# Kernel optimization log

Hardware: AMD Instinct MI355X
Metric: run time of the kernel (lower is better)

## Reference

```python
import jax
import jax.numpy as jnp
import numpy as np

KSIZE, STRIDE, RATE, FUSE_K, SCALE = 3, 1, 2, 3, 10.0
ESCAPE_NAN = 1e-4


def _same_pad(x, k, s):
    # replicates torch same_padding: asymmetric zero pad so out = ceil(H/s)
    H, W = x.shape[2], x.shape[3]
    oh, ow = -(-H // s), -(-W // s)
    ph = max(0, (oh - 1) * s + k - H)
    pw = max(0, (ow - 1) * s + k - W)
    return jnp.pad(x, ((0, 0), (0, 0), (ph // 2, ph - ph // 2), (pw // 2, pw - pw // 2)))


def _extract_patches(x, k, s):
    # torch extract_image_patches: -> [B, L, C, k, k] with L = out_h*out_w
    x = _same_pad(x, k, s)
    B, C, H, W = x.shape
    Ho, Wo = (H - k) // s + 1, (W - k) // s + 1
    slices = [x[:, :, i:i + Ho * s:s, j:j + Wo * s:s] for i in range(k) for j in range(k)]
    p = jnp.stack(slices, axis=2).reshape(B, C, k, k, Ho, Wo)
    return p.transpose(0, 4, 5, 1, 2, 3).reshape(B, Ho * Wo, C, k, k)


def _contextual_attention(f, b, mask):
    dn = ('NCHW', 'OIHW', 'NCHW')
    # raw background patches for the final deconv: k = 2*rate, stride = rate
    raw_pat = _extract_patches(b, 2 * RATE, RATE * STRIDE)  # [B, L, C, 4, 4]
    # nearest-neighbor 1/rate downsample (torch F.interpolate nearest, sf=0.5)
    f_ds = f[:, :, ::RATE, ::RATE]
    b_ds = b[:, :, ::RATE, ::RATE]
    m_ds = mask[:, :, ::RATE, ::RATE]
    B, C, Hf, Wf = f_ds.shape
    Hb, Wb = b_ds.shape[2], b_ds.shape[3]
    b_pat = _extract_patches(b_ds, KSIZE, STRIDE)  # [B, L, C, 3, 3], L = Hb*Wb
    m_pat = _extract_patches(m_ds, KSIZE, STRIDE)[0]  # [L, 1, 3, 3] (first sample only, as in torch)
    mm = (jnp.mean(m_pat, axis=(1, 2, 3)) == 0.0).astype(f.dtype)[None, :, None, None]  # [1, L, 1, 1]
    fuse_w = jnp.eye(FUSE_K, dtype=f.dtype).reshape(1, 1, FUSE_K, FUSE_K)

    def per_item(xi, wi, raw_wi):
        # xi: [C,Hf,Wf]; wi: [L,C,3,3]; raw_wi: [L,C,4,4]
        max_wi = jnp.sqrt(jnp.sum(wi * wi + ESCAPE_NAN, axis=(1, 2, 3), keepdims=True))
        wi_n = wi / max_wi
        # matching conv: scores [1, L, Hf, Wf]
        yi = jax.lax.conv_general_dilated(xi[None], wi_n, (1, 1), ((1, 1), (1, 1)), dimension_numbers=dn)
        # fuse: identity-diagonal 3x3 conv along (bg_idx, fg_idx) twice with transposes
        yi = yi.reshape(1, 1, Hb * Wb, Hf * Wf)
        yi = jax.lax.conv_general_dilated(yi, fuse_w, (1, 1), ((1, 1), (1, 1)), dimension_numbers=dn)
        yi = yi.reshape(Hb, Wb, Hf, Wf).transpose(1, 0, 3, 2).reshape(1, 1, Hb * Wb, Hf * Wf)
        yi = jax.lax.conv_general_dilated(yi, fuse_w, (1, 1), ((1, 1), (1, 1)), dimension_numbers=dn)
        yi = yi.reshape(Wb, Hb, Wf, Hf).transpose(1, 0, 3, 2).reshape(1, Hb * Wb, Hf, Wf)
        yi = yi * mm
        yi = jax.nn.softmax(yi * SCALE, axis=1) * mm
        # conv_transpose2d(yi, raw_wi[I=L,O=C], stride=rate, padding=1) / 4
        w2 = jnp.flip(raw_wi, (2, 3)).transpose(1, 0, 2, 3)  # [C, L, 4, 4]
        pad = 2 * RATE - 1 - 1  # k - 1 - torch_padding = 2
        out = jax.lax.conv_general_dilated(yi, w2, (1, 1), ((pad, pad), (pad, pad)),
                                           lhs_dilation=(RATE, RATE), dimension_numbers=dn) / 4.0
        return out[0]

    return jax.vmap(per_item)(f_ds, b_pat, raw_pat)  # [B, C, H, W]


def setup_inputs() -> dict:
    key = jax.random.key(0)
    k1, k2 = jax.random.split(key)
    B, C, H, W = 2, 128, 128, 128
    f = jax.random.normal(k1, (B, C, H, W), dtype=jnp.float32)
    b = jax.random.normal(k2, (B, C, H, W), dtype=jnp.float32)
    mask = jnp.zeros((B, 1, H, W), dtype=jnp.float32)
    return {"f": f, "b": b, "mask": mask}


def reference(f, b, mask):
    return _contextual_attention(f, b, mask)
```

## Files before the change

kernel.cpp:

```cpp
#include <hip/hip_runtime.h>
#include <math.h>

#define CDIM 128
#define HF   128
#define WF   128
#define NP   4096
#define NCHUNK 64

typedef __attribute__((ext_vector_type(8))) short short8;
typedef __attribute__((ext_vector_type(16))) float f16a;
typedef float __attribute__((ext_vector_type(4), aligned(16))) f4a16;
typedef float __attribute__((ext_vector_type(4), aligned(4)))  f4u;

__device__ inline ushort f2bf(float x) {
  union { float f; unsigned u; } v; v.f = x;
  unsigned r = v.u + 0x7fff + ((v.u >> 16) & 1);
  return (ushort)(r >> 16);
}
__device__ inline float bf2f(ushort h) {
  union { unsigned u; float f; } v; v.u = ((unsigned)h) << 16; return v.f;
}

__device__ inline void gl2lds16(const ushort* g, ushort* l) {
  __builtin_amdgcn_global_load_lds((const __attribute__((address_space(1))) void*)g,
                                   (__attribute__((address_space(3))) void*)l, 16, 0, 0);
}

__global__ __launch_bounds__(256) void k_prep(const float* __restrict__ f,
                                              const float* __restrict__ b,
                                              ushort* __restrict__ fcat,
                                              ushort* __restrict__ bcat,
                                              float* __restrict__ s2) {
  int idx = blockIdx.x * 256 + threadIdx.x;
  int c = idx & 127, pos = idx >> 7;
  int x = pos & 63, y = pos >> 6;
  int src = c * 16384 + y * 256 + x * 2;
  float fv = f[src], bv = b[src];
  ushort fh = f2bf(fv); ushort fl = f2bf(fv - bf2f(fh));
  ushort bh = f2bf(bv); ushort bl = f2bf(bv - bf2f(bh));
  size_t base = (size_t)pos * 384;
  fcat[base + c] = fh; fcat[base + 128 + c] = fl; fcat[base + 256 + c] = fh;
  bcat[base + c] = bh; bcat[base + 128 + c] = bh; bcat[base + 256 + c] = bl;
  float sq = bv * bv;
#pragma unroll
  for (int off = 32; off; off >>= 1) sq += __shfl_down(sq, off);
  __shared__ float wsum[4];
  if ((threadIdx.x & 63) == 0) wsum[threadIdx.x >> 6] = sq;
  __syncthreads();
  if (threadIdx.x == 0) s2[blockIdx.x * 2]     = wsum[0] + wsum[1];
  if (threadIdx.x == 1) s2[blockIdx.x * 2 + 1] = wsum[2] + wsum[3];
}

__global__ __launch_bounds__(256) void k_mmpnorm(const float* __restrict__ mask,
                                                 const float* __restrict__ s2,
                                                 float* __restrict__ mmp,
                                                 float* __restrict__ rnrm) {
  int bx = blockIdx.x, t = threadIdx.x;
  if (bx < 16) {
    int a = bx * 256 + t;
    int yb = a & 63, xb = a >> 6;
    float s = 0.f;
    for (int dy = -1; dy <= 1; ++dy)
      for (int dx = -1; dx <= 1; ++dx) {
        int y = yb + dy, x = xb + dx;
        if ((unsigned)y < 64u && (unsigned)x < 64u)
          s += mask[y * 256 + x * 2];
      }
    mmp[a] = (s == 0.0f) ? 1.0f : 0.0f;
  } else {
    int p = (bx - 16) * 256 + t;
    int xb = p & 63, yb = p >> 6;
    float s = 0.f;
    for (int dy = -1; dy <= 1; ++dy)
      for (int dx = -1; dx <= 1; ++dx) {
        int y = yb + dy, x = xb + dx;
        if ((unsigned)y < 64u && (unsigned)x < 64u) s += s2[y * 64 + x];
      }
    rnrm[p] = rsqrtf(s + 1152.0f * 1.0e-4f);
  }
}

__global__ __launch_bounds__(512) void k_mfma_gemm(const ushort* __restrict__ A,
                                                   const ushort* __restrict__ B,
                                                   float* __restrict__ Out,
                                                   int Kdim, int lda, int ldb, int ldo) {
  __shared__ ushort As[3][256 * 64];
  __shared__ ushort Bs[3][128 * 64];
  const int tid = threadIdx.x;
  const int wave = tid >> 6, lane = tid & 63;
  const int l32 = lane & 31, khalf = lane >> 5;
  const int m0 = blockIdx.y * 256, n0 = blockIdx.x * 128;
  const int wm = (wave >> 1) * 64, wn = (wave & 1) * 64;
  const int srow = lane >> 3;
  const int gperm = ((lane & 7) ^ srow) * 8;

  const ushort* Ag = A + (size_t)(m0 + wave * 8 + srow) * lda + gperm;
  const ushort* Bg = B + (size_t)(n0 + wave * 8 + srow) * ldb + gperm;
  ushort* AsW = &As[0][0] + (wave * 8) * 64;
  ushort* BsW = &Bs[0][0] + (wave * 8) * 64;

#define STG_A(bufi, tt, q) gl2lds16(Ag + (size_t)((q) * 64) * lda + ((tt) << 6), \
                                    AsW + (bufi) * 16384 + (q) * 4096)
#define STG_B(bufi, tt, q) gl2lds16(Bg + (size_t)((q) * 64) * ldb + ((tt) << 6), \
                                    BsW + (bufi) * 8192 + (q) * 4096)

  f16a acc[2][2];
#pragma unroll
  for (int i = 0; i < 2; ++i)
#pragma unroll
    for (int j = 0; j < 2; ++j)
#pragma unroll
      for (int r = 0; r < 16; ++r) acc[i][j][r] = 0.f;

  const int NT = Kdim >> 6;

  STG_A(0, 0, 0); STG_B(0, 0, 0); STG_A(0, 0, 1); STG_B(0, 0, 1); STG_A(0, 0, 2); STG_A(0, 0, 3);
  STG_A(1, 1, 0); STG_B(1, 1, 0); STG_A(1, 1, 1); STG_B(1, 1, 1); STG_A(1, 1, 2); STG_A(1, 1, 3);
  asm volatile("s_waitcnt vmcnt(6)");
  __builtin_amdgcn_s_barrier();

  int cb = 0, sb = 2;
  for (int t = 0; t < NT; ++t) {
    const ushort* Ar = &As[cb][0];
    const ushort* Br = &Bs[cb][0];
    const bool st = (t + 2) < NT;
    const int tn = t + 2;
#pragma unroll
    for (int h = 0; h < 2; ++h) {
      short8 af[2][2], bf[2][2];
#pragma unroll
      for (int ss = 0; ss < 2; ++ss) {
        const int s = h * 2 + ss;
#pragma unroll
        for (int u = 0; u < 2; ++u) {
          int am = wm + u * 32 + l32;
          int ga = ((s * 2 + khalf) ^ (am & 7)) * 8;
          af[ss][u] = *reinterpret_cast<const short8*>(&Ar[am * 64 + ga]);
          int bn = wn + u * 32 + l32;
          int gb = ((s * 2 + khalf) ^ (bn & 7)) * 8;
          bf[ss][u] = *reinterpret_cast<const short8*>(&Br[bn * 64 + gb]);
        }
      }
      if (st) {
        if (h == 0) { STG_A(sb, tn, 0); STG_B(sb, tn, 0); STG_A(sb, tn, 1); }
        else        { STG_B(sb, tn, 1); STG_A(sb, tn, 2); STG_A(sb, tn, 3); }
      }
      __builtin_amdgcn_s_barrier();
      asm volatile("s_waitcnt lgkmcnt(0)");
      __builtin_amdgcn_s_setprio(1);
#pragma unroll
      for (int ss = 0; ss < 2; ++ss) {
        acc[0][0] = __builtin_amdgcn_mfma_f32_32x32x16_bf16(af[ss][0], bf[ss][0], acc[0][0], 0, 0, 0);
        acc[0][1] = __builtin_amdgcn_mfma_f32_32x32x16_bf16(af[ss][0], bf[ss][1], acc[0][1], 0, 0, 0);
        acc[1][0] = __builtin_amdgcn_mfma_f32_32x32x16_bf16(af[ss][1], bf[ss][0], acc[1][0], 0, 0, 0);
        acc[1][1] = __builtin_amdgcn_mfma_f32_32x32x16_bf16(af[ss][1], bf[ss][1], acc[1][1], 0, 0, 0);
      }
      __builtin_amdgcn_s_setprio(0);
      if (h == 1) asm volatile("s_waitcnt vmcnt(6)");
      __builtin_amdgcn_s_barrier();
    }
    cb = (cb == 2) ? 0 : cb + 1;
    sb = (sb == 2) ? 0 : sb + 1;
  }

#pragma unroll
  for (int i = 0; i < 2; ++i)
#pragma unroll
    for (int j = 0; j < 2; ++j)
#pragma unroll
      for (int r = 0; r < 16; ++r) {
        int row = (r & 3) + 8 * (r >> 2) + 4 * khalf;
        Out[(size_t)(m0 + wm + i * 32 + row) * ldo + (n0 + wn + j * 32 + l32)] = acc[i][j][r];
      }
#undef STG_A
#undef STG_B
}

__global__ __launch_bounds__(256) void k_s0(const float* __restrict__ D,
                                            const float* __restrict__ rnrm,
                                            float* __restrict__ S0) {
  int p = blockIdx.x;
  int yb = p >> 6, xb = p & 63;
  float rp = rnrm[p];
  int t = threadIdx.x;
#pragma unroll
  for (int it = 0; it < 4; ++it) {
    int q = (it * 256 + t) << 2;
    int qy = q >> 6, qx = q & 63;
    f4a16 acc = (f4a16){0.f, 0.f, 0.f, 0.f};
#pragma unroll
    for (int dy = -1; dy <= 1; ++dy) {
      if ((unsigned)(yb + dy) >= 64u) continue;
      if ((unsigned)(qy + dy) >= 64u) continue;
#pragma unroll
      for (int dx = -1; dx <= 1; ++dx) {
        if ((unsigned)(xb + dx) >= 64u) continue;
        int delta = dy * 64 + dx;
        const float* base = D + (size_t)(p + delta) * 4096;
        f4u v;
        if (dx == -1 && qx == 0) {
          f4u r = *(const f4u*)(base + q + delta + 1);
          v = (f4u){0.f, r.x, r.y, r.z};
        } else {
          v = *(const f4u*)(base + q + delta);
          if (dx == 1 && qx == 60) v.w = 0.f;
        }
        acc += v;
      }
    }
    acc *= rp;
    *(f4a16*)(S0 + ((size_t)p << 12) + q) = acc;
  }
}

__global__ __launch_bounds__(256) void k_fuse1(const float* __restrict__ S0,
                                               float* __restrict__ Yp) {
  __shared__ float row[4160];
  int i = blockIdx.x;
  int t = threadIdx.x;
  const float* r0 = S0 + (size_t)(i - 1) * 4096;
  const float* r1 = S0 + (size_t)i * 4096;
  const float* r2 = S0 + (size_t)(i + 1) * 4096;
  bool up = (i > 0), dn = (i < 4095);
#pragma unroll
  for (int jj = 0; jj < 4; ++jj) {
    int j = (jj * 256 + t) << 2;
    f4u s = *(const f4u*)(r1 + j);
    if (up) {
      f4u a;
      if (j == 0) { f4u r = *(const f4u*)r0; a = (f4u){0.f, r.x, r.y, r.z}; }
      else a = *(const f4u*)(r0 + j - 1);
      s += a;
    }
    if (dn) {
      f4u d = *(const f4u*)(r2 + j + 1);
      if (j == 4092) d.w = 0.f;
      s += d;
    }
    int base = j + (j >> 6);
    row[base + 0] = s.x; row[base + 1] = s.y; row[base + 2] = s.z; row[base + 3] = s.w;
  }
  __syncthreads();
  int a = ((i & 63) << 6) | (i >> 6);
  float* orow = Yp + ((size_t)a << 12);
#pragma unroll
  for (int bb = 0; bb < 4; ++bb) {
    int b4 = (bb * 256 + t) << 2;
    f4a16 o;
#pragma unroll
    for (int k = 0; k < 4; ++k) {
      int jT = (((b4 + k) & 63) << 6) | ((b4 + k) >> 6);
      o[k] = row[jT + (jT >> 6)];
    }
    *(f4a16*)(orow + b4) = o;
  }
}

__global__ __launch_bounds__(256) void k_smax_part(const float* __restrict__ Yp,
                                                   const float* __restrict__ mmp,
                                                   float* __restrict__ pm,
                                                   float* __restrict__ ps) {
  int v = (blockIdx.x * 256 + threadIdx.x) << 2;
  int chunk = blockIdx.y;
  f4a16 m = (f4a16){-1e30f, -1e30f, -1e30f, -1e30f};
  f4a16 s = (f4a16){0.f, 0.f, 0.f, 0.f};
  int u0 = chunk * (4096 / NCHUNK);
  for (int u = u0; u < u0 + (4096 / NCHUNK); ++u) {
    const float* row = Yp + ((size_t)u << 12);
    f4u tv = *(const f4u*)(row + v);
    if (u > 0) {
      f4u a;
      if (v == 0) { f4u r = *(const f4u*)(row - 4096); a = (f4u){0.f, r.x, r.y, r.z}; }
      else a = *(const f4u*)(row - 4096 + v - 1);
      tv += a;
    }
    if (u < 4095) {
      f4u d = *(const f4u*)(row + 4096 + v + 1);
      if (v == 4092) d.w = 0.f;
      tv += d;
    }
    float g = 10.0f * mmp[u];
    f4u x = tv * g;
#pragma unroll
    for (int l = 0; l < 4; ++l) {
      float xl = x[l];
      if (xl > m[l]) { s[l] = s[l] * __expf(m[l] - xl) + 1.0f; m[l] = xl; }
      else           { s[l] += __expf(xl - m[l]); }
    }
  }
  *(f4a16*)(pm + chunk * NP + v) = m;
  *(f4a16*)(ps + chunk * NP + v) = s;
}

__global__ __launch_bounds__(256) void k_epilogue(const float* __restrict__ Yp,
                                                  const float* __restrict__ pm,
                                                  const float* __restrict__ ps,
                                                  const float* __restrict__ mmp,
                                                  ushort* __restrict__ AT,
                                                  const float* __restrict__ bimg,
                                                  ushort* __restrict__ VtT) {
  __shared__ float T[64][65];
  __shared__ float pmS[4][64];
  __shared__ float psS[4][64];
  __shared__ float mS[64];
  __shared__ float rsS[64];
  int gx = blockIdx.x;
  int t = threadIdx.x;
  if (gx < 4096) {
    int a0 = (gx & 63) * 64, b0 = (gx >> 6) * 64;
    int j = t & 63, grp = t >> 6;
    float m = -1e30f, s = 0.f;
    for (int ch = grp * 16; ch < grp * 16 + 16; ++ch) {
      float m2 = pm[ch * NP + b0 + j], s2 = ps[ch * NP + b0 + j];
      if (m2 > m) { s = s * __expf(m - m2) + s2; m = m2; }
      else        { s += s2 * __expf(m2 - m); }
    }
    pmS[grp][j] = m; psS[grp][j] = s;
    __syncthreads();
    if (grp == 0) {
      for (int g2 = 1; g2 < 4; ++g2) {
        float m2 = pmS[g2][j], s2 = psS[g2][j];
        if (m2 > m) { s = s * __expf(m - m2) + s2; m = m2; }
        else        { s += s2 * __expf(m2 - m); }
      }
      mS[j] = m; rsS[j] = 1.0f / s;
    }
    __syncthreads();
    int i = t >> 4, j4 = (t & 15) << 2;
    f4a16 mc = *(const f4a16*)&mS[j4];
    f4a16 rs = *(const f4a16*)&rsS[j4];
#pragma unroll
    for (int r = 0; r < 4; ++r) {
      int al = r * 16 + i;
      int a = a0 + al;
      const float* row = Yp + ((size_t)a << 12);
      int b = b0 + j4;
      f4u y = *(const f4u*)(row + b);
      if (a > 0) {
        f4u u_;
        if (b == 0) { f4u rr = *(const f4u*)(row - 4096); u_ = (f4u){0.f, rr.x, rr.y, rr.z}; }
        else u_ = *(const f4u*)(row - 4096 + b - 1);
        y += u_;
      }
      if (a < 4095) {
        f4u d = *(const f4u*)(row + 4096 + b + 1);
        if (b == 4092) d.w = 0.f;
        y += d;
      }
      float g = mmp[a];
      f4u x = y * (10.0f * g);
#pragma unroll
      for (int l = 0; l < 4; ++l)
        T[al][j4 + l] = g * __expf(x[l] - mc[l]) * rs[l];
    }
    __syncthreads();
    int by0 = b0 >> 6;
    int cgrp = (t & 7) * 8;
#pragma unroll
    for (int pass = 0; pass < 2; ++pass) {
      int bl = pass * 32 + (t >> 3);
      int q = bl * 64 + by0;
      uint4 w;
      w.x = (unsigned)f2bf(T[cgrp + 0][bl]) | ((unsigned)f2bf(T[cgrp + 1][bl]) << 16);
      w.y = (unsigned)f2bf(T[cgrp + 2][bl]) | ((unsigned)f2bf(T[cgrp + 3][bl]) << 16);
      w.z = (unsigned)f2bf(T[cgrp + 4][bl]) | ((unsigned)f2bf(T[cgrp + 5][bl]) << 16);
      w.w = (unsigned)f2bf(T[cgrp + 6][bl]) | ((unsigned)f2bf(T[cgrp + 7][bl]) << 16);
      *(uint4*)(AT + ((size_t)q << 12) + a0 + cgrp) = w;
    }
  } else {
    int k2 = gx - 4096;
    int c = k2 >> 4, dy = (k2 >> 2) & 3, dx = k2 & 3;
    int px = t & 63;
#pragma unroll
    for (int r = 0; r < 16; ++r) {
      int py = r * 4 + (t >> 6);
      int sy = 2 * py + dy - 1, sx = 2 * px + dx - 1;
      float v = 0.f;
      if ((unsigned)sy < (unsigned)HF && (unsigned)sx < (unsigned)WF)
        v = bimg[c * 16384 + sy * 128 + sx];
      T[py][px] = v;
    }
    __syncthreads();
    ushort* orow = VtT + (size_t)k2 * 4096;
#pragma unroll
    for (int r = 0; r < 16; ++r) {
      int a = r * 256 + t;
      orow[a] = f2bf(T[a & 63][a >> 6]);
    }
  }
}

__global__ __launch_bounds__(256) void k_scatter(const float* __restrict__ M,
                                                 float* __restrict__ out) {
  int idx = blockIdx.x * 256 + threadIdx.x;
  int ox = idx & 127, oy = (idx >> 7) & 127, c = idx >> 14;
  int qy[2], dyv[2], qx[2], dxv[2];
  if (oy & 1) { qy[0] = (oy - 1) >> 1; dyv[0] = 2; qy[1] = (oy + 1) >> 1; dyv[1] = 0; }
  else        { qy[0] = (oy >> 1) - 1; dyv[0] = 3; qy[1] = oy >> 1;       dyv[1] = 1; }
  if (ox & 1) { qx[0] = (ox - 1) >> 1; dxv[0] = 2; qx[1] = (ox + 1) >> 1; dxv[1] = 0; }
  else        { qx[0] = (ox >> 1) - 1; dxv[0] = 3; qx[1] = ox >> 1;       dxv[1] = 1; }
  float s = 0.f;
#pragma unroll
  for (int i = 0; i < 2; ++i) {
    if ((unsigned)qy[i] >= 64u) continue;
#pragma unroll
    for (int j = 0; j < 2; ++j) {
      if ((unsigned)qx[j] >= 64u) continue;
      int k = c * 16 + dyv[i] * 4 + dxv[j];
      s += M[(size_t)k * NP + qy[i] * 64 + qx[j]];
    }
  }
  out[idx] = 0.25f * s;
}

extern "C" void kernel_launch(void* const* d_in, const int* in_sizes, int n_in,
                              void* d_out, int out_size, void* d_ws, size_t ws_size,
                              hipStream_t stream) {
  const float* f_all = (const float*)d_in[0];
  const float* b_all = (const float*)d_in[1];
  const float* m_all = (const float*)d_in[2];
  float* out = (float*)d_out;

  float* ws = (float*)d_ws;
  float* bufD = ws;
  float* bufS = ws + 16777216;
  ushort* fcat = (ushort*)bufS;
  ushort* bcat = (ushort*)(bufS + 786432);
  float* S0  = bufS;
  float* Yp  = bufD;
  ushort* AT  = (ushort*)bufS;
  ushort* VtT = (ushort*)(bufS + 8388608);
  float* Mbuf = bufD;
  float* smalls = ws + 2 * 16777216;
  float* s2    = smalls;
  float* rnrm  = s2 + 4096;
  float* mmp   = rnrm + 4096;
  float* pm    = mmp + 4096;
  float* ps    = pm + NCHUNK * NP;

  const size_t zsF = (size_t)CDIM * HF * WF;
  const size_t zsM = (size_t)HF * WF;

  for (int it = 0; it < 2; ++it) {
    const float* f = f_all + it * zsF;
    const float* b = b_all + it * zsF;
    const float* mk = m_all + it * zsM;
    float* o = out + it * zsF;

    k_prep<<<2048, 256, 0, stream>>>(f, b, fcat, bcat, s2);
    k_mmpnorm<<<32, 256, 0, stream>>>(mk, s2, mmp, rnrm);
    k_mfma_gemm<<<dim3(32, 16), 512, 0, stream>>>(bcat, fcat, bufD, 384, 384, 384, NP);
    k_s0<<<4096, 256, 0, stream>>>(bufD, rnrm, S0);
    k_fuse1<<<4096, 256, 0, stream>>>(S0, Yp);
    k_smax_part<<<dim3(4, NCHUNK), 256, 0, stream>>>(Yp, mmp, pm, ps);
    k_epilogue<<<6144, 256, 0, stream>>>(Yp, pm, ps, mmp, AT, b, VtT);
    k_mfma_gemm<<<dim3(32, 8), 512, 0, stream>>>(VtT, AT, Mbuf, NP, NP, NP, NP);
    k_scatter<<<8192, 256, 0, stream>>>(Mbuf, o);
  }
}
```

Measured before the change: 669.6 us.

## Enlarge GEMM tile to 256x256, double-buffer LDS, split-K the second GEMM

The MFMA GEMM tile grows from 256x128 to 256x256, with each wave computing a 128x64 sub-tile (4x2 accumulators) instead of 64x64. LDS staging moves from a triple buffer to a double buffer, and fragment reads for the next k-step are interleaved with the MFMAs. The second GEMM (K=4096) is split in two along K via blockIdx.z, and the scatter kernel sums the two partial outputs. The aim is more data reuse per LDS load and enough blocks in flight for the smaller grid, at the cost of higher register pressure, less prefetch depth, and an extra partial-result buffer that scatter must read.

```diff
diff --git a/kernel.cpp b/kernel.cpp
--- a/kernel.cpp
+++ b/kernel.cpp
@@ -83,94 +83,111 @@
 __global__ __launch_bounds__(512) void k_mfma_gemm(const ushort* __restrict__ A,
                                                    const ushort* __restrict__ B,
                                                    float* __restrict__ Out,
-                                                   int Kdim, int lda, int ldb, int ldo) {
-  __shared__ ushort As[3][256 * 64];
-  __shared__ ushort Bs[3][128 * 64];
+                                                   int Kdim, int lda, int ldb, int ldo,
+                                                   long osplit) {
+  __shared__ ushort As[2][256 * 64];
+  __shared__ ushort Bs[2][256 * 64];
   const int tid = threadIdx.x;
   const int wave = tid >> 6, lane = tid & 63;
   const int l32 = lane & 31, khalf = lane >> 5;
-  const int m0 = blockIdx.y * 256, n0 = blockIdx.x * 128;
-  const int wm = (wave >> 1) * 64, wn = (wave & 1) * 64;
+  const int m0 = blockIdx.y * 256, n0 = blockIdx.x * 256;
+  const int wm = (wave >> 2) * 128, wn = (wave & 3) * 64;
   const int srow = lane >> 3;
   const int gperm = ((lane & 7) ^ srow) * 8;
+
+  const int koff = blockIdx.z * Kdim;
+  A += koff; B += koff;
+  Out += (size_t)blockIdx.z * osplit;
 
   const ushort* Ag = A + (size_t)(m0 + wave * 8 + srow) * lda + gperm;
   const ushort* Bg = B + (size_t)(n0 + wave * 8 + srow) * ldb + gperm;
   ushort* AsW = &As[0][0] + (wave * 8) * 64;
   ushort* BsW = &Bs[0][0] + (wave * 8) * 64;
 
-#define STG_A(bufi, tt, q) gl2lds16(Ag + (size_t)((q) * 64) * lda + ((tt) << 6), \
-                                    AsW + (bufi) * 16384 + (q) * 4096)
-#define STG_B(bufi, tt, q) gl2lds16(Bg + (size_t)((q) * 64) * ldb + ((tt) << 6), \
-                                    BsW + (bufi) * 8192 + (q) * 4096)
-
-  f16a acc[2][2];
-#pragma unroll
-  for (int i = 0; i < 2; ++i)
-#pragma unroll
-    for (int j = 0; j < 2; ++j)
-#pragma unroll
-      for (int r = 0; r < 16; ++r) acc[i][j][r] = 0.f;
+#define STG_A(sl, tt, q) gl2lds16(Ag + (size_t)((q) * 64) * lda + ((tt) << 6), \
+                                  AsW + (sl) * 16384 + (q) * 4096)
+#define STG_B(sl, tt, q) gl2lds16(Bg + (size_t)((q) * 64) * ldb + ((tt) << 6), \
+                                  BsW + (sl) * 16384 + (q) * 4096)
+
+  f16a acc[4][2];
+#pragma unroll
+  for (int u = 0; u < 4; ++u)
+#pragma unroll
+    for (int v = 0; v < 2; ++v)
+#pragma unroll
+      for (int r = 0; r < 16; ++r) acc[u][v][r] = 0.f;
 
   const int NT = Kdim >> 6;
 
-  STG_A(0, 0, 0); STG_B(0, 0, 0); STG_A(0, 0, 1); STG_B(0, 0, 1); STG_A(0, 0, 2); STG_A(0, 0, 3);
-  STG_A(1, 1, 0); STG_B(1, 1, 0); STG_A(1, 1, 1); STG_B(1, 1, 1); STG_A(1, 1, 2); STG_A(1, 1, 3);
-  asm volatile("s_waitcnt vmcnt(6)");
+#pragma unroll
+  for (int q = 0; q < 4; ++q) { STG_A(0, 0, q); STG_B(0, 0, q); }
+  if (NT > 1) {
+#pragma unroll
+    for (int q = 0; q < 4; ++q) { STG_A(1, 1, q); STG_B(1, 1, q); }
+    asm volatile("s_waitcnt vmcnt(8)" ::: "memory");
+  } else {
+    asm volatile("s_waitcnt vmcnt(0)" ::: "memory");
+  }
   __builtin_amdgcn_s_barrier();
 
-  int cb = 0, sb = 2;
   for (int t = 0; t < NT; ++t) {
-    const ushort* Ar = &As[cb][0];
-    const ushort* Br = &Bs[cb][0];
-    const bool st = (t + 2) < NT;
-    const int tn = t + 2;
-#pragma unroll
-    for (int h = 0; h < 2; ++h) {
-      short8 af[2][2], bf[2][2];
-#pragma unroll
-      for (int ss = 0; ss < 2; ++ss) {
-        const int s = h * 2 + ss;
-#pragma unroll
-        for (int u = 0; u < 2; ++u) {
-          int am = wm + u * 32 + l32;
-          int ga = ((s * 2 + khalf) ^ (am & 7)) * 8;
-          af[ss][u] = *reinterpret_cast<const short8*>(&Ar[am * 64 + ga]);
-          int bn = wn + u * 32 + l32;
-          int gb = ((s * 2 + khalf) ^ (bn & 7)) * 8;
-          bf[ss][u] = *reinterpret_cast<const short8*>(&Br[bn * 64 + gb]);
+    const int sl = t & 1;
+    const ushort* Ar = &As[sl][0];
+    const ushort* Br = &Bs[sl][0];
+    short8 af[2][4], bf[2][2];
+
+#define FRAG_READS(sidx) do { \
+  _Pragma("unroll") for (int u = 0; u < 4; ++u) { \
+    int am = wm + u * 32 + l32; \
+    int ga = (((sidx) * 2 + khalf) ^ (am & 7)) * 8; \
+    af[(sidx) & 1][u] = *reinterpret_cast<const short8*>(&Ar[am * 64 + ga]); } \
+  _Pragma("unroll") for (int v = 0; v < 2; ++v) { \
+    int bn = wn + v * 32 + l32; \
+    int gb = (((sidx) * 2 + khalf) ^ (bn & 7)) * 8; \
+    bf[(sidx) & 1][v] = *reinterpret_cast<const short8*>(&Br[bn * 64 + gb]); } \
+} while (0)
+
+    FRAG_READS(0);
+#pragma unroll
+    for (int s = 0; s < 4; ++s) {
+      if (s == 1) FRAG_READS(2);
+      if (s == 2) FRAG_READS(3);
+      if (s == 0) FRAG_READS(1);
+      if (s == 3) {
+        asm volatile("s_waitcnt lgkmcnt(0)" ::: "memory");
+        __builtin_amdgcn_sched_barrier(0);
+        __builtin_amdgcn_s_barrier();
+        __builtin_amdgcn_sched_barrier(0);
+        if (t + 2 < NT) {
+#pragma unroll
+          for (int q = 0; q < 4; ++q) { STG_A(sl, t + 2, q); STG_B(sl, t + 2, q); }
         }
-      }
-      if (st) {
-        if (h == 0) { STG_A(sb, tn, 0); STG_B(sb, tn, 0); STG_A(sb, tn, 1); }
-        else        { STG_B(sb, tn, 1); STG_A(sb, tn, 2); STG_A(sb, tn, 3); }
-      }
+        __builtin_amdgcn_s_setprio(1);
+      }
+#pragma unroll
+      for (int u = 0; u < 4; ++u)
+#pragma unroll
+        for (int v = 0; v < 2; ++v)
+          acc[u][v] = __builtin_amdgcn_mfma_f32_32x32x16_bf16(af[s & 1][u], bf[s & 1][v],
+                                                              acc[u][v], 0, 0, 0);
+      if (s == 3) __builtin_amdgcn_s_setprio(0);
+    }
+    if (t + 1 < NT) {
+      if (t + 2 < NT) asm volatile("s_waitcnt vmcnt(8)" ::: "memory");
+      else            asm volatile("s_waitcnt vmcnt(0)" ::: "memory");
       __builtin_amdgcn_s_barrier();
-      asm volatile("s_waitcnt lgkmcnt(0)");
-      __builtin_amdgcn_s_setprio(1);
-#pragma unroll
-      for (int ss = 0; ss < 2; ++ss) {
-        acc[0][0] = __builtin_amdgcn_mfma_f32_32x32x16_bf16(af[ss][0], bf[ss][0], acc[0][0], 0, 0, 0);
-        acc[0][1] = __builtin_amdgcn_mfma_f32_32x32x16_bf16(af[ss][0], bf[ss][1], acc[0][1], 0, 0, 0);
-        acc[1][0] = __builtin_amdgcn_mfma_f32_32x32x16_bf16(af[ss][1], bf[ss][0], acc[1][0], 0, 0, 0);
-        acc[1][1] = __builtin_amdgcn_mfma_f32_32x32x16_bf16(af[ss][1], bf[ss][1], acc[1][1], 0, 0, 0);
-      }
-      __builtin_amdgcn_s_setprio(0);
-      if (h == 1) asm volatile("s_waitcnt vmcnt(6)");
-      __builtin_amdgcn_s_barrier();
-    }
-    cb = (cb == 2) ? 0 : cb + 1;
-    sb = (sb == 2) ? 0 : sb + 1;
-  }
-
-#pragma unroll
-  for (int i = 0; i < 2; ++i)
-#pragma unroll
-    for (int j = 0; j < 2; ++j)
+    }
+#undef FRAG_READS
+  }
+
+#pragma unroll
+  for (int u = 0; u < 4; ++u)
+#pragma unroll
+    for (int v = 0; v < 2; ++v)
 #pragma unroll
       for (int r = 0; r < 16; ++r) {
         int row = (r & 3) + 8 * (r >> 2) + 4 * khalf;
-        Out[(size_t)(m0 + wm + i * 32 + row) * ldo + (n0 + wn + j * 32 + l32)] = acc[i][j][r];
+        Out[(size_t)(m0 + wm + u * 32 + row) * ldo + (n0 + wn + v * 32 + l32)] = acc[u][v][r];
       }
 #undef STG_A
 #undef STG_B
@@ -390,7 +407,8 @@
   }
 }
 
-__global__ __launch_bounds__(256) void k_scatter(const float* __restrict__ M,
+__global__ __launch_bounds__(256) void k_scatter(const float* __restrict__ Ma,
+                                                 const float* __restrict__ Mb,
                                                  float* __restrict__ out) {
   int idx = blockIdx.x * 256 + threadIdx.x;
   int ox = idx & 127, oy = (idx >> 7) & 127, c = idx >> 14;
@@ -407,7 +425,8 @@
     for (int j = 0; j < 2; ++j) {
       if ((unsigned)qx[j] >= 64u) continue;
       int k = c * 16 + dyv[i] * 4 + dxv[j];
-      s += M[(size_t)k * NP + qy[i] * 64 + qx[j]];
+      size_t off = (size_t)k * NP + qy[i] * 64 + qx[j];
+      s += Ma[off] + Mb[off];
     }
   }
   out[idx] = 0.25f * s;
@@ -430,7 +449,8 @@
   float* Yp  = bufD;
   ushort* AT  = (ushort*)bufS;
   ushort* VtT = (ushort*)(bufS + 8388608);
-  float* Mbuf = bufD;
+  float* M0 = bufD;
+  float* M1 = bufD + 8388608;
   float* smalls = ws + 2 * 16777216;
   float* s2    = smalls;
   float* rnrm  = s2 + 4096;
@@ -449,12 +469,13 @@
 
     k_prep<<<2048, 256, 0, stream>>>(f, b, fcat, bcat, s2);
     k_mmpnorm<<<32, 256, 0, stream>>>(mk, s2, mmp, rnrm);
-    k_mfma_gemm<<<dim3(32, 16), 512, 0, stream>>>(bcat, fcat, bufD, 384, 384, 384, NP);
+    k_mfma_gemm<<<dim3(16, 16, 1), 512, 0, stream>>>(bcat, fcat, bufD, 384, 384, 384, NP, 0);
     k_s0<<<4096, 256, 0, stream>>>(bufD, rnrm, S0);
     k_fuse1<<<4096, 256, 0, stream>>>(S0, Yp);
     k_smax_part<<<dim3(4, NCHUNK), 256, 0, stream>>>(Yp, mmp, pm, ps);
     k_epilogue<<<6144, 256, 0, stream>>>(Yp, pm, ps, mmp, AT, b, VtT);
-    k_mfma_gemm<<<dim3(32, 8), 512, 0, stream>>>(VtT, AT, Mbuf, NP, NP, NP, NP);
-    k_scatter<<<8192, 256, 0, stream>>>(Mbuf, o);
-  }
-}
+    k_mfma_gemm<<<dim3(16, 8, 2), 512, 0, stream>>>(VtT, AT, M0, 2048, NP, NP, NP,
+                                                    (long)2048 * 4096);
+    k_scatter<<<8192, 256, 0, stream>>>(M0, M1, o);
+  }
+}
```

New measurement: 652.4 us. 1.03x faster.
